# Kernel optimization log

Measured on AMD Instinct MI355X. Metric: run time of the kernel, lower is better.

The kernel has to match this reference:

```python
import jax, jax.numpy as jnp
import numpy as np

B, N, D, H, C = 2, 2048, 1024, 16, 3
Dh = D // H


def setup_inputs() -> dict:
    key = jax.random.key(0)
    ks = jax.random.split(key, 6)
    x = jax.random.normal(ks[0], (B, N, D), jnp.float32)
    coords = jax.random.normal(ks[1], (B, N, C), jnp.float32)
    attn_mask = jax.random.normal(ks[2], (N, N), jnp.float32) * 0.1  # additive float bias (2d kind)
    Wqkv = jax.random.normal(ks[3], (D, 3 * D), jnp.float32) / np.sqrt(D)
    bqkv = jax.random.normal(ks[4], (3 * D,), jnp.float32) * 0.01
    rel_weight = jax.random.normal(ks[5], (H, C), jnp.float32) * 0.02
    return {"x": x, "coords": coords, "attn_mask": attn_mask,
            "Wqkv": Wqkv, "bqkv": bqkv, "rel_weight": rel_weight}


def reference(x, coords, attn_mask, Wqkv, bqkv, rel_weight):
    b, n, d = x.shape
    h, dh = rel_weight.shape[0], d // rel_weight.shape[0]
    scale = 1.0 / np.sqrt(float(dh))

    qkv = x @ Wqkv + bqkv                      # [B,N,3D]
    q, k, v = jnp.split(qkv, 3, axis=-1)

    def to_heads(t):
        return t.reshape(b, n, h, dh).transpose(0, 2, 1, 3)  # [B,H,N,Dh]

    qh, kh, vh = to_heads(q), to_heads(k), to_heads(v)

    # scaled dot-product scores (flex_attention applies scale before score_mod)
    scores = jnp.einsum('bhnd,bhmd->bhnm', qh, kh) * scale   # [B,H,N,N]

    # coordinate-derived per-head relative bias: coord_proj[b,h,qi] - coord_proj[b,h,kj]
    coord_proj = jnp.einsum('bnc,hc->bhn', coords.astype(jnp.float32), rel_weight)
    scores = scores + coord_proj[:, :, :, None] - coord_proj[:, :, None, :]

    # additive float mask bias, '2d' kind: shape (N,N) broadcast over B,H
    scores = scores + attn_mask[None, None, :, :]

    attn = jax.nn.softmax(scores, axis=-1)
    out = jnp.einsum('bhnm,bhmd->bhnd', attn, vh)            # [B,H,N,Dh]
    return out.transpose(0, 2, 1, 3).reshape(b, n, d)        # [B,N,D]
```

## Files before the change

### kernel.cpp

```cpp
#include <hip/hip_runtime.h>

typedef _Float16 half8 __attribute__((ext_vector_type(8)));
typedef _Float16 half4 __attribute__((ext_vector_type(4)));
typedef _Float16 half2v __attribute__((ext_vector_type(2)));
typedef float floatx4 __attribute__((ext_vector_type(4)));

#define LOG2E 1.44269504088896f
#define QSCALE 0.18033688011112f

__device__ __forceinline__ void async16(const void* g, void* l) {
    __builtin_amdgcn_global_load_lds(
        (const __attribute__((address_space(1))) unsigned int*)g,
        (__attribute__((address_space(3))) unsigned int*)l, 16, 0, 0);
}
__device__ __forceinline__ half4 pack4(float a, float b, float c, float d) {
    half2v lo = __builtin_bit_cast(half2v, __builtin_amdgcn_cvt_pkrtz(a, b));
    half2v hi = __builtin_bit_cast(half2v, __builtin_amdgcn_cvt_pkrtz(c, d));
    half4 r; r[0] = lo[0]; r[1] = lo[1]; r[2] = hi[0]; r[3] = hi[1];
    return r;
}

__global__ __launch_bounds__(256) void k_prep(
    const float* __restrict__ x, const float* __restrict__ W,
    const float* __restrict__ coords, const float* __restrict__ rw,
    const float* __restrict__ mask,
    _Float16* __restrict__ xh, _Float16* __restrict__ Wt,
    _Float16* __restrict__ esch, _Float16* __restrict__ maskp) {
    __shared__ float smem[4352];
    int bx = blockIdx.x, tid = threadIdx.x;
    if (bx < 2048) {
        int i = bx * 256 + tid;
        const floatx4* xin = (const floatx4*)x;
        floatx4 a = xin[i * 2];
        floatx4 b = xin[i * 2 + 1];
        half8 h;
        h[0] = (_Float16)a[0]; h[1] = (_Float16)a[1]; h[2] = (_Float16)a[2]; h[3] = (_Float16)a[3];
        h[4] = (_Float16)b[0]; h[5] = (_Float16)b[1]; h[6] = (_Float16)b[2]; h[7] = (_Float16)b[3];
        *(half8*)&xh[i * 8] = h;
    } else if (bx < 5120) {
        int b2 = bx - 2048;
        int n0 = (b2 % 96) * 32, k0 = (b2 / 96) * 32;
        int tx = tid & 31, ty = tid >> 5;
        float (*tile)[33] = (float(*)[33])smem;
        #pragma unroll
        for (int r = 0; r < 4; ++r)
            tile[ty + r * 8][tx] = W[(size_t)(k0 + ty + r * 8) * 3072 + n0 + tx];
        __syncthreads();
        #pragma unroll
        for (int r = 0; r < 4; ++r)
            Wt[(size_t)(n0 + ty + r * 8) * 1024 + k0 + tx] = (_Float16)tile[tx][ty + r * 8];
    } else if (bx < 5376) {
        int idx = (bx - 5120) * 256 + tid;
        int bh = idx >> 11, n = idx & 2047;
        int b = bh >> 4, h = bh & 15;
        const float* c = &coords[(b * 2048 + n) * 3];
        const float* w = &rw[h * 3];
        float v = -LOG2E * (c[0] * w[0] + c[1] * w[1] + c[2] * w[2]);
        esch[idx] = (_Float16)__builtin_amdgcn_exp2f(v);
    } else {
        int bid = bx - 5376;
        int qt = bid >> 5, kt = bid & 31;
        int row0 = qt * 64, col0 = kt * 64;
        int lr = tid >> 2, lc = (tid & 3) * 16;
        #pragma unroll
        for (int j = 0; j < 4; ++j)
            *(floatx4*)&smem[lr * 68 + lc + j * 4] =
                *(const floatx4*)&mask[(size_t)(row0 + lr) * 2048 + col0 + lc + j * 4];
        __syncthreads();
        int w = tid >> 6, lane = tid & 63, quad = lane >> 4, l16 = lane & 15;
        half4* outp = (half4*)maskp + (size_t)((qt * 32 + kt) * 4 + w) * 256 + lane;
        #pragma unroll
        for (int t = 0; t < 4; ++t) {
            floatx4 m = *(const floatx4*)&smem[(w * 16 + l16) * 68 + t * 16 + quad * 4];
            outp[t * 64] = pack4(m[0] * LOG2E, m[1] * LOG2E, m[2] * LOG2E, m[3] * LOG2E);
        }
    }
}

__global__ __launch_bounds__(256) void k_gemm(
    const _Float16* __restrict__ Ah, const _Float16* __restrict__ Bt,
    const float* __restrict__ bias, const _Float16* __restrict__ esch,
    _Float16* __restrict__ qh, _Float16* __restrict__ kh, _Float16* __restrict__ vt) {
    __shared__ _Float16 smem[16384];
    int tid = threadIdx.x;
    int w = tid >> 6, lane = tid & 63;
    int quad = lane >> 4, l16 = lane & 15;
    int m0 = blockIdx.y * 128;
    int n0 = blockIdx.x * 128;
    bool QK = n0 < 2048;
    int mq = (w >> 1) * 64, nq = (w & 1) * 64;
    int c0 = n0 + nq;

    int rl4 = lane >> 2;
    int pb4 = lane & 3;
    floatx4 acc[4][4] = {};

    const _Float16* ap[2];
    const _Float16* bp[2];
    #pragma unroll
    for (int j = 0; j < 2; ++j) {
        int row = w * 32 + j * 16 + rl4;
        int lb = pb4 ^ (row & 3) ^ ((row >> 2) & 3);
        ap[j] = Ah + (size_t)(m0 + row) * 1024 + lb * 8;
        bp[j] = Bt + (size_t)(n0 + row) * 1024 + lb * 8;
    }

    #define GSTAGE(buf) {                                      \
        _Float16* As_ = smem + (buf) * 8192;                   \
        _Float16* Bs_ = As_ + 4096;                            \
        async16(ap[0], &As_[(w * 32) * 32]);                   \
        async16(ap[1], &As_[(w * 32 + 16) * 32]);              \
        async16(bp[0], &Bs_[(w * 32) * 32]);                   \
        async16(bp[1], &Bs_[(w * 32 + 16) * 32]);              \
        ap[0] += 32; ap[1] += 32; bp[0] += 32; bp[1] += 32;    \
    }

    #define GBODY(cur, last) {                                                         \
        __syncthreads();                                                               \
        if (!(last)) GSTAGE((cur) ^ 1);                                                \
        const _Float16* As_ = smem + (cur) * 8192;                                     \
        const _Float16* Bs_ = As_ + 4096;                                              \
        half8 af[4], bf[4];                                                            \
        _Pragma("unroll")                                                              \
        for (int s = 0; s < 4; ++s) {                                                  \
            int ra = mq + s * 16 + l16;                                                \
            af[s] = *(const half8*)&As_[ra * 32 +                                      \
                ((quad ^ (ra & 3) ^ ((ra >> 2) & 3)) << 3)];                           \
            int rb = nq + s * 16 + l16;                                                \
            bf[s] = *(const half8*)&Bs_[rb * 32 +                                      \
                ((quad ^ (rb & 3) ^ ((rb >> 2) & 3)) << 3)];                           \
        }                                                                              \
        if (QK) {                                                                      \
            _Pragma("unroll")                                                          \
            for (int ms = 0; ms < 4; ++ms)                                             \
                _Pragma("unroll")                                                      \
                for (int ns = 0; ns < 4; ++ns)                                         \
                    acc[ms][ns] = __builtin_amdgcn_mfma_f32_16x16x32_f16(              \
                        bf[ns], af[ms], acc[ms][ns], 0, 0, 0);                         \
        } else {                                                                       \
            _Pragma("unroll")                                                          \
            for (int ms = 0; ms < 4; ++ms)                                             \
                _Pragma("unroll")                                                      \
                for (int ns = 0; ns < 4; ++ns)                                         \
                    acc[ms][ns] = __builtin_amdgcn_mfma_f32_16x16x32_f16(              \
                        af[ms], bf[ns], acc[ms][ns], 0, 0, 0);                         \
        }                                                                              \
    }

    GSTAGE(0);
    #pragma unroll 1
    for (int kt2 = 0; kt2 < 15; ++kt2) {
        GBODY(0, false);
        GBODY(1, false);
    }
    GBODY(0, false);
    GBODY(1, true);
    #undef GBODY
    #undef GSTAGE

    __syncthreads();

    _Float16* Ls = smem + w * 2304;
    int rl = lane >> 3, pb = lane & 7;
    int b = (m0 + mq) >> 11, nbase = (m0 + mq) & 2047;
    if (QK) {
        float qsc = (c0 < 1024) ? QSCALE : 1.0f;
        int h2 = c0 >> 6;
        _Float16* dst = (h2 < 16 ? qh : kh) + (size_t)(((b << 4) + (h2 & 15)) * 2048) * 64;
        int d0 = pb << 3;
        #pragma unroll
        for (int p = 0; p < 2; ++p) {
            #pragma unroll
            for (int ns = 0; ns < 4; ++ns) {
                floatx4 b4 = *(const floatx4*)&bias[c0 + ns * 16 + quad * 4];
                #pragma unroll
                for (int m2 = 0; m2 < 2; ++m2) {
                    int ms = p * 2 + m2;
                    floatx4 v;
                    #pragma unroll
                    for (int i = 0; i < 4; ++i) v[i] = (acc[ms][ns][i] + b4[i]) * qsc;
                    *(half4*)&Ls[(m2 * 16 + l16) * 72 + ns * 16 + quad * 4] =
                        pack4(v[0], v[1], v[2], v[3]);
                }
            }
            #pragma unroll
            for (int rep = 0; rep < 4; ++rep) {
                int nl = rep * 8 + rl;
                half8 v = *(const half8*)&Ls[nl * 72 + d0];
                *(half8*)&dst[(size_t)(nbase + p * 32 + nl) * 64 + d0] = v;
            }
        }
    } else {
        int h = (c0 - 2048) >> 6;
        _Float16* dst = vt + (size_t)(((b << 4) + h) * 64) * 2048;
        const _Float16* ePtr = esch + (size_t)((b << 4) + h) * 2048 + nbase + quad * 4;
        float ef[4][4];
        #pragma unroll
        for (int ms = 0; ms < 4; ++ms) {
            half4 e4 = *(const half4*)&ePtr[ms * 16];
            #pragma unroll
            for (int i = 0; i < 4; ++i) ef[ms][i] = (float)e4[i];
        }
        int noff = pb << 3;
        #pragma unroll
        for (int p = 0; p < 2; ++p) {
            #pragma unroll
            for (int n2 = 0; n2 < 2; ++n2) {
                int ns = p * 2 + n2;
                float bv = bias[c0 + ns * 16 + l16];
                #pragma unroll
                for (int ms = 0; ms < 4; ++ms) {
                    *(half4*)&Ls[(n2 * 16 + l16) * 72 + ms * 16 + quad * 4] =
                        pack4((acc[ms][ns][0] + bv) * ef[ms][0],
                              (acc[ms][ns][1] + bv) * ef[ms][1],
                              (acc[ms][ns][2] + bv) * ef[ms][2],
                              (acc[ms][ns][3] + bv) * ef[ms][3]);
                }
            }
            #pragma unroll
            for (int rep = 0; rep < 4; ++rep) {
                int cl = rep * 8 + rl;
                half8 v = *(const half8*)&Ls[cl * 72 + noff];
                *(half8*)&dst[(size_t)(p * 32 + cl) * 2048 + nbase + noff] = v;
            }
        }
    }
}

__global__ __launch_bounds__(256, 2) void k_attn(
    const _Float16* __restrict__ qh, const _Float16* __restrict__ kh,
    const _Float16* __restrict__ vt, const _Float16* __restrict__ maskp,
    const _Float16* __restrict__ esch, float* __restrict__ out) {
    __shared__ _Float16 KV[2][8192];
    int tid = threadIdx.x;
    int w = tid >> 6, lane = tid & 63;
    int quad = lane >> 4, l16 = lane & 15;
    int rl = lane >> 3, pb = lane & 7;
    int bid = blockIdx.x;
    int qt2 = bid & 15, bh = bid >> 4;
    int b = bh >> 4, h = bh & 15;
    int qrow = qt2 * 128 + w * 32;

    half8 qf[2][2];
    #pragma unroll
    for (int g = 0; g < 2; ++g) {
        const _Float16* qp = &qh[((size_t)bh * 2048 + qrow + g * 16 + l16) * 64];
        qf[g][0] = *(const half8*)&qp[quad * 8];
        qf[g][1] = *(const half8*)&qp[32 + quad * 8];
    }
    floatx4 o0[4] = {}, o1[4] = {};
    floatx4 ol0 = {}, ol1 = {};

    int sw = (pb ^ rl) << 3;
    const _Float16* kp0 = kh + (size_t)bh * 131072 + (size_t)(w * 16 + rl) * 64 + sw;
    const _Float16* kp1 = kp0 + 512;
    const _Float16* vp0 = vt + (size_t)bh * 131072 + (size_t)(w * 16 + rl) * 2048 + sw;
    const _Float16* vp1 = vp0 + 16384;
    const half4* mp0 = (const half4*)maskp +
        ((size_t)(qt2 * 2 + (w >> 1)) * 128 + (w & 1) * 2) * 256 + lane;
    const half4* mp1 = mp0 + 256;
    const _Float16* ep = esch + bh * 2048 + quad * 4;

    half4 mA0[4], mA1[4], eA[4];
    half4 mB0[4], mB1[4], eB[4];

    #define STAGE(buf) {                                             \
        async16(kp0, &KV[buf][(w * 16) * 64]);                       \
        async16(kp1, &KV[buf][(w * 16 + 8) * 64]);                   \
        async16(vp0, &KV[buf][4096 + (w * 16) * 64]);                \
        async16(vp1, &KV[buf][4096 + (w * 16 + 8) * 64]);            \
        kp0 += 4096; kp1 += 4096; vp0 += 64; vp1 += 64;              \
    }

    #define MPREF(M0, M1, EV) {                                      \
        _Pragma("unroll")                                            \
        for (int t = 0; t < 4; ++t) M0[t] = mp0[t * 64];             \
        _Pragma("unroll")                                            \
        for (int t = 0; t < 4; ++t) M1[t] = mp1[t * 64];             \
        _Pragma("unroll")                                            \
        for (int t = 0; t < 4; ++t) EV[t] = *(const half4*)&ep[t * 16]; \
        mp0 += 1024; mp1 += 1024; ep += 64;                          \
    }

    #define BODY(cur, last, MC0, MC1, EC, MN0, MN1, EN) {                              \
        __syncthreads();                                                               \
        if (!(last)) { STAGE((cur) ^ 1); MPREF(MN0, MN1, EN); }                        \
        const _Float16* Ksc = &KV[cur][0];                                             \
        const _Float16* Vsc = &KV[cur][4096];                                          \
        half8 kf0[4], kf1[4];                                                          \
        _Pragma("unroll")                                                              \
        for (int t = 0; t < 4; ++t) {                                                  \
            int r = t * 16 + l16;                                                      \
            kf0[t] = *(const half8*)&Ksc[r * 64 + ((quad ^ (r & 7)) << 3)];            \
            kf1[t] = *(const half8*)&Ksc[r * 64 + (((quad + 4) ^ (r & 7)) << 3)];      \
        }                                                                              \
        half4 pt[2][4];                                                                \
        _Pragma("unroll")                                                              \
        for (int t = 0; t < 4; ++t) {                                                  \
            half4 ml = MC0[t];                                                         \
            floatx4 z;                                                                 \
            z[0] = (float)ml[0]; z[1] = (float)ml[1];                                  \
            z[2] = (float)ml[2]; z[3] = (float)ml[3];                                  \
            z = __builtin_amdgcn_mfma_f32_16x16x32_f16(kf0[t], qf[0][0], z, 0, 0, 0);  \
            z = __builtin_amdgcn_mfma_f32_16x16x32_f16(kf1[t], qf[0][1], z, 0, 0, 0);  \
            pt[0][t] = pack4(__builtin_amdgcn_exp2f(z[0]),                             \
                             __builtin_amdgcn_exp2f(z[1]),                             \
                             __builtin_amdgcn_exp2f(z[2]),                             \
                             __builtin_amdgcn_exp2f(z[3]));                            \
        }                                                                              \
        _Pragma("unroll")                                                              \
        for (int t = 0; t < 4; ++t) {                                                  \
            half4 ml = MC1[t];                                                         \
            floatx4 z;                                                                 \
            z[0] = (float)ml[0]; z[1] = (float)ml[1];                                  \
            z[2] = (float)ml[2]; z[3] = (float)ml[3];                                  \
            z = __builtin_amdgcn_mfma_f32_16x16x32_f16(kf0[t], qf[1][0], z, 0, 0, 0);  \
            z = __builtin_amdgcn_mfma_f32_16x16x32_f16(kf1[t], qf[1][1], z, 0, 0, 0);  \
            pt[1][t] = pack4(__builtin_amdgcn_exp2f(z[0]),                             \
                             __builtin_amdgcn_exp2f(z[1]),                             \
                             __builtin_amdgcn_exp2f(z[2]),                             \
                             __builtin_amdgcn_exp2f(z[3]));                            \
        }                                                                              \
        _Pragma("unroll")                                                              \
        for (int t = 0; t < 4; ++t) {                                                  \
            ol0 = __builtin_amdgcn_mfma_f32_16x16x16f16(EC[t], pt[0][t], ol0, 0, 0, 0); \
            ol1 = __builtin_amdgcn_mfma_f32_16x16x16f16(EC[t], pt[1][t], ol1, 0, 0, 0); \
        }                                                                              \
        _Pragma("unroll")                                                              \
        for (int dt = 0; dt < 4; ++dt) {                                               \
            int rv = dt * 16 + l16;                                                    \
            _Pragma("unroll")                                                          \
            for (int t = 0; t < 4; ++t) {                                              \
                half4 vf = *(const half4*)&Vsc[rv * 64 +                               \
                    (((t * 2 + (quad >> 1)) ^ (rv & 7)) << 3) + ((quad & 1) << 2)];    \
                o0[dt] = __builtin_amdgcn_mfma_f32_16x16x16f16(vf, pt[0][t], o0[dt], 0, 0, 0); \
                o1[dt] = __builtin_amdgcn_mfma_f32_16x16x16f16(vf, pt[1][t], o1[dt], 0, 0, 0); \
            }                                                                          \
        }                                                                              \
    }

    STAGE(0);
    MPREF(mA0, mA1, eA);
    #pragma unroll 1
    for (int kt2 = 0; kt2 < 15; ++kt2) {
        BODY(0, false, mA0, mA1, eA, mB0, mB1, eB);
        BODY(1, false, mB0, mB1, eB, mA0, mA1, eA);
    }
    BODY(0, false, mA0, mA1, eA, mB0, mB1, eB);
    BODY(1, true,  mB0, mB1, eB, mA0, mA1, eA);
    #undef BODY
    #undef MPREF
    #undef STAGE

    float inv0 = 1.f / ol0[0];
    float inv1 = 1.f / ol1[0];
    size_t obase = ((size_t)(b * 2048 + qrow + l16)) * 1024 + h * 64 + quad * 4;
    #pragma unroll
    for (int dt = 0; dt < 4; ++dt) {
        floatx4 r0, r1;
        #pragma unroll
        for (int i = 0; i < 4; ++i) { r0[i] = o0[dt][i] * inv0; r1[i] = o1[dt][i] * inv1; }
        *(floatx4*)&out[obase + dt * 16] = r0;
        *(floatx4*)&out[obase + (size_t)16 * 1024 + dt * 16] = r1;
    }
}

extern "C" void kernel_launch(void* const* d_in, const int* in_sizes, int n_in,
                              void* d_out, int out_size, void* d_ws, size_t ws_size,
                              hipStream_t stream) {
    const float* x      = (const float*)d_in[0];
    const float* coords = (const float*)d_in[1];
    const float* mask   = (const float*)d_in[2];
    const float* Wqkv   = (const float*)d_in[3];
    const float* bqkv   = (const float*)d_in[4];
    const float* rw     = (const float*)d_in[5];
    float* out = (float*)d_out;

    char* ws = (char*)d_ws;
    _Float16* xh    = (_Float16*)(ws);
    _Float16* maskp = (_Float16*)(ws + 8388608);
    _Float16* Wt    = (_Float16*)(ws + 16777216);
    _Float16* qh    = (_Float16*)(ws + 23068672);
    _Float16* kh    = (_Float16*)(ws + 31457280);
    _Float16* vt    = (_Float16*)(ws + 39845888);
    _Float16* esch  = (_Float16*)(ws + 48234496);

    k_prep<<<6400, 256, 0, stream>>>(x, Wqkv, coords, rw, mask, xh, Wt, esch, maskp);
    k_gemm<<<dim3(24, 32), 256, 0, stream>>>(xh, Wt, bqkv, esch, qh, kh, vt);
    k_attn<<<512, 256, 0, stream>>>(qh, kh, vt, maskp, esch, out);
}
```

Before: 197.6 us.

## Split attention KV range across two wave groups per block and combine in LDS

```diff
diff --git a/kernel.cpp b/kernel.cpp
--- a/kernel.cpp
+++ b/kernel.cpp
@@ -227,19 +227,20 @@
     }
 }
 
-__global__ __launch_bounds__(256, 2) void k_attn(
+__global__ __launch_bounds__(512, 4) void k_attn(
     const _Float16* __restrict__ qh, const _Float16* __restrict__ kh,
     const _Float16* __restrict__ vt, const _Float16* __restrict__ maskp,
     const _Float16* __restrict__ esch, float* __restrict__ out) {
-    __shared__ _Float16 KV[2][8192];
+    __shared__ _Float16 KV[2][2][8192];
     int tid = threadIdx.x;
     int w = tid >> 6, lane = tid & 63;
+    int g2 = w >> 2, wg = w & 3;
     int quad = lane >> 4, l16 = lane & 15;
     int rl = lane >> 3, pb = lane & 7;
     int bid = blockIdx.x;
     int qt2 = bid & 15, bh = bid >> 4;
     int b = bh >> 4, h = bh & 15;
-    int qrow = qt2 * 128 + w * 32;
+    int qrow = qt2 * 128 + wg * 32;
 
     half8 qf[2][2];
     #pragma unroll
@@ -252,23 +253,25 @@
     floatx4 ol0 = {}, ol1 = {};
 
     int sw = (pb ^ rl) << 3;
-    const _Float16* kp0 = kh + (size_t)bh * 131072 + (size_t)(w * 16 + rl) * 64 + sw;
+    const _Float16* kp0 = kh + (size_t)bh * 131072 + (size_t)(wg * 16 + rl) * 64 + sw
+                             + (size_t)g2 * 65536;
     const _Float16* kp1 = kp0 + 512;
-    const _Float16* vp0 = vt + (size_t)bh * 131072 + (size_t)(w * 16 + rl) * 2048 + sw;
+    const _Float16* vp0 = vt + (size_t)bh * 131072 + (size_t)(wg * 16 + rl) * 2048 + sw
+                             + (size_t)g2 * 1024;
     const _Float16* vp1 = vp0 + 16384;
     const half4* mp0 = (const half4*)maskp +
-        ((size_t)(qt2 * 2 + (w >> 1)) * 128 + (w & 1) * 2) * 256 + lane;
+        ((size_t)(qt2 * 2 + (wg >> 1)) * 128 + (size_t)g2 * 64 + (wg & 1) * 2) * 256 + lane;
     const half4* mp1 = mp0 + 256;
-    const _Float16* ep = esch + bh * 2048 + quad * 4;
+    const _Float16* ep = esch + bh * 2048 + g2 * 1024 + quad * 4;
 
     half4 mA0[4], mA1[4], eA[4];
     half4 mB0[4], mB1[4], eB[4];
 
     #define STAGE(buf) {                                             \
-        async16(kp0, &KV[buf][(w * 16) * 64]);                       \
-        async16(kp1, &KV[buf][(w * 16 + 8) * 64]);                   \
-        async16(vp0, &KV[buf][4096 + (w * 16) * 64]);                \
-        async16(vp1, &KV[buf][4096 + (w * 16 + 8) * 64]);            \
+        async16(kp0, &KV[g2][buf][(wg * 16) * 64]);                  \
+        async16(kp1, &KV[g2][buf][(wg * 16 + 8) * 64]);              \
+        async16(vp0, &KV[g2][buf][4096 + (wg * 16) * 64]);           \
+        async16(vp1, &KV[g2][buf][4096 + (wg * 16 + 8) * 64]);       \
         kp0 += 4096; kp1 += 4096; vp0 += 64; vp1 += 64;              \
     }
 
@@ -285,8 +288,8 @@
     #define BODY(cur, last, MC0, MC1, EC, MN0, MN1, EN) {                              \
         __syncthreads();                                                               \
         if (!(last)) { STAGE((cur) ^ 1); MPREF(MN0, MN1, EN); }                        \
-        const _Float16* Ksc = &KV[cur][0];                                             \
-        const _Float16* Vsc = &KV[cur][4096];                                          \
+        const _Float16* Ksc = &KV[g2][cur][0];                                         \
+        const _Float16* Vsc = &KV[g2][cur][4096];                                      \
         half8 kf0[4], kf1[4];                                                          \
         _Pragma("unroll")                                                              \
         for (int t = 0; t < 4; ++t) {                                                  \
@@ -342,7 +345,7 @@
     STAGE(0);
     MPREF(mA0, mA1, eA);
     #pragma unroll 1
-    for (int kt2 = 0; kt2 < 15; ++kt2) {
+    for (int kt2 = 0; kt2 < 7; ++kt2) {
         BODY(0, false, mA0, mA1, eA, mB0, mB1, eB);
         BODY(1, false, mB0, mB1, eB, mA0, mA1, eA);
     }
@@ -352,16 +355,60 @@
     #undef MPREF
     #undef STAGE
 
-    float inv0 = 1.f / ol0[0];
-    float inv1 = 1.f / ol1[0];
-    size_t obase = ((size_t)(b * 2048 + qrow + l16)) * 1024 + h * 64 + quad * 4;
-    #pragma unroll
-    for (int dt = 0; dt < 4; ++dt) {
-        floatx4 r0, r1;
-        #pragma unroll
-        for (int i = 0; i < 4; ++i) { r0[i] = o0[dt][i] * inv0; r1[i] = o1[dt][i] * inv1; }
-        *(floatx4*)&out[obase + dt * 16] = r0;
-        *(floatx4*)&out[obase + (size_t)16 * 1024 + dt * 16] = r1;
+    __syncthreads();
+    float* comb = (float*)KV;
+    {
+        float* dst = comb + ((size_t)w * 17) * 64 + lane;
+        if (g2 == 0) {
+            #pragma unroll
+            for (int dt = 0; dt < 4; ++dt)
+                #pragma unroll
+                for (int i = 0; i < 4; ++i)
+                    dst[(dt * 4 + i) * 64] = o1[dt][i];
+            dst[16 * 64] = ol1[0];
+        } else {
+            #pragma unroll
+            for (int dt = 0; dt < 4; ++dt)
+                #pragma unroll
+                for (int i = 0; i < 4; ++i)
+                    dst[(dt * 4 + i) * 64] = o0[dt][i];
+            dst[16 * 64] = ol0[0];
+        }
+    }
+    __syncthreads();
+    {
+        const float* src = comb + ((size_t)(w ^ 4) * 17) * 64 + lane;
+        if (g2 == 0) {
+            #pragma unroll
+            for (int dt = 0; dt < 4; ++dt)
+                #pragma unroll
+                for (int i = 0; i < 4; ++i)
+                    o0[dt][i] += src[(dt * 4 + i) * 64];
+            float inv = 1.f / (ol0[0] + src[16 * 64]);
+            size_t obase = ((size_t)(b * 2048 + qrow + l16)) * 1024 + h * 64 + quad * 4;
+            #pragma unroll
+            for (int dt = 0; dt < 4; ++dt) {
+                floatx4 r;
+                #pragma unroll
+                for (int i = 0; i < 4; ++i) r[i] = o0[dt][i] * inv;
+                *(floatx4*)&out[obase + dt * 16] = r;
+            }
+        } else {
+            #pragma unroll
+            for (int dt = 0; dt < 4; ++dt)
+                #pragma unroll
+                for (int i = 0; i < 4; ++i)
+                    o1[dt][i] += src[(dt * 4 + i) * 64];
+            float inv = 1.f / (ol1[0] + src[16 * 64]);
+            size_t obase = ((size_t)(b * 2048 + qrow + 16 + l16)) * 1024 + h * 64 + quad * 4;
+            #pragma unroll
+            for (int dt = 0; dt < 4; ++dt) {
+                floatx4 r;
+                #pragma unroll
+                for (int i = 0; i < 4; ++i) r[i] = o1[dt][i] * inv;
+                *(floatx4*)&out[obase + dt * 16] = r;
+            }
+        }
     }
 }
 
@@ -387,5 +434,5 @@
 
     k_prep<<<6400, 256, 0, stream>>>(x, Wqkv, coords, rw, mask, xh, Wt, esch, maskp);
     k_gemm<<<dim3(24, 32), 256, 0, stream>>>(xh, Wt, bqkv, esch, qh, kh, vt);
-    k_attn<<<512, 256, 0, stream>>>(qh, kh, vt, maskp, esch, out);
-}
+    k_attn<<<512, 512, 0, stream>>>(qh, kh, vt, maskp, esch, out);
+}
```

Measured after the change: 223.5 us. +13.1%, slower.
